# Performance work log

Measured on AMD Instinct MI355X. Metric: run time of the kernel, lower is better.

## Reference

```python
import jax, jax.numpy as jnp
import numpy as np

B, TQ, TK, N = 4, 128, 512, 1024   # batch, query len, key len, key_size
QS, VS, OS = 1024, 1024, 1024      # query_size, value_size, output_size


def setup_inputs() -> dict:
    key = jax.random.key(0)
    ks = jax.random.split(key, 9)
    s_q = 1.0 / np.sqrt(QS)
    s_k = 1.0 / np.sqrt(N)
    s_o = 1.0 / np.sqrt(QS + VS)
    return {
        "query": jax.random.normal(ks[0], (B, TQ, QS), jnp.float32),
        "keys": jax.random.normal(ks[1], (B, TK, N), jnp.float32),
        "values": jax.random.normal(ks[2], (B, TK, VS), jnp.float32),
        # linear_q: query_size -> key_size
        "Wq": jax.random.normal(ks[3], (N, QS), jnp.float32) * s_q,
        "bq": jax.random.normal(ks[4], (N,), jnp.float32) * s_q,
        # linear_att: key_size -> 1
        "w_att": jax.random.normal(ks[5], (N,), jnp.float32) * s_k,
        "b_att": jax.random.normal(ks[6], (), jnp.float32) * s_k,
        # linear_out: (query_size + value_size) -> output_size
        "Wout": jax.random.normal(ks[7], (OS, QS + VS), jnp.float32) * s_o,
        "bout": jax.random.normal(ks[8], (OS,), jnp.float32) * s_o,
    }


def reference(query, keys, values, Wq, bq, w_att, b_att, Wout, bout):
    # linear_q: [b, t_q, query_size] -> [b, t_q, n]
    att_query = jnp.einsum("bqe,ne->bqn", query, Wq) + bq
    # Bahdanau additive score: tanh(q + k) then linear_att (n -> 1)
    # intermediate is [b, t_q, t_k, n] as in the original module
    sum_qk = jnp.tanh(att_query[:, :, None, :] + keys[:, None, :, :])
    scores = jnp.einsum("bqkn,n->bqk", sum_qk, w_att) + b_att  # [b, t_q, t_k]
    scores_normalized = jax.nn.softmax(scores, axis=2)
    # context = softmax(scores) @ values  (dropout is identity with p=0)
    context = jnp.einsum("bqk,bkv->bqv", scores_normalized, values)
    # linear_out on concat([query, context]) + tanh
    cat = jnp.concatenate([query, context], axis=2)  # [b, t_q, q+v]
    out = jnp.tanh(jnp.einsum("bqc,oc->bqo", cat, Wout) + bout)
    return out, scores_normalized
```

## Files before the change

kernel.cpp:

```cpp
#include <hip/hip_runtime.h>
#include <math.h>

static constexpr int B_  = 4;
static constexpr int TQ  = 128;
static constexpr int TK  = 512;
static constexpr int NN  = 1024;
static constexpr int QS  = 1024;
static constexpr int VS  = 1024;
static constexpr int OS  = 1024;

#define K2F    2.8853900817779268f
#define LOG2EF 1.4426950408889634f

typedef __attribute__((ext_vector_type(8))) short bf16x8;
typedef __attribute__((ext_vector_type(4))) float f32x4;

#define MFMA16(a,b,c) __builtin_amdgcn_mfma_f32_16x16x32_bf16((a),(b),(c),0,0,0)

__device__ __forceinline__ ushort bf16_rne(float x) {
    uint u = __float_as_uint(x);
    u += 0x7FFFu + ((u >> 16) & 1u);
    return (ushort)(u >> 16);
}
__device__ __forceinline__ void split2(float x, ushort& h, ushort& l) {
    ushort hh = bf16_rne(x);
    float hv = __uint_as_float((uint)hh << 16);
    h = hh;
    l = bf16_rne(x - hv);
}

__global__ __launch_bounds__(256) void cvt_all_kernel(
    const float* __restrict__ Q, const float* __restrict__ Wq,
    const float* __restrict__ Wo, const float* __restrict__ V,
    ushort* __restrict__ Qh, ushort* __restrict__ Ql,
    ushort* __restrict__ Wqh, ushort* __restrict__ Wql,
    ushort* __restrict__ Woh, ushort* __restrict__ Wol,
    ushort* __restrict__ Vth, ushort* __restrict__ Vtl)
{
    __shared__ float tile[64][65];
    const int bid = blockIdx.x;
    const int t = threadIdx.x;
    if (bid < 3584) {
        const float* src; ushort *h, *l; int idx;
        if (bid < 512)       { src = Q;  h = Qh;  l = Ql;  idx = bid*256 + t; }
        else if (bid < 1536) { src = Wq; h = Wqh; l = Wql; idx = (bid-512)*256 + t; }
        else                 { src = Wo; h = Woh; l = Wol; idx = (bid-1536)*256 + t; }
        float4 v = ((const float4*)src)[idx];
        ushort4 hh, ll;
        split2(v.x, hh.x, ll.x); split2(v.y, hh.y, ll.y);
        split2(v.z, hh.z, ll.z); split2(v.w, hh.w, ll.w);
        ((ushort4*)h)[idx] = hh;
        ((ushort4*)l)[idx] = ll;
        return;
    }
    const int vid = bid - 3584;
    const int v0 = (vid & 15) * 64;
    const int k0 = ((vid >> 4) & 7) * 64;
    const int b  = vid >> 7;
    const float* src = V + ((size_t)b*TK + k0)*VS + v0;
    #pragma unroll
    for (int p = 0; p < 4; ++p) {
        int r = (t >> 4) + p*16, c = (t & 15) * 4;
        float4 vv = *(const float4*)(src + (size_t)r*VS + c);
        tile[r][c] = vv.x; tile[r][c+1] = vv.y; tile[r][c+2] = vv.z; tile[r][c+3] = vv.w;
    }
    __syncthreads();
    ushort* dh = Vth + (size_t)b*(VS*TK) + (size_t)v0*TK + k0;
    ushort* dl = Vtl + (size_t)b*(VS*TK) + (size_t)v0*TK + k0;
    #pragma unroll
    for (int p = 0; p < 4; ++p) {
        int vr = (t >> 4) + p*16, kc = (t & 15) * 4;
        ushort4 hh, ll;
        split2(tile[kc+0][vr], hh.x, ll.x);
        split2(tile[kc+1][vr], hh.y, ll.y);
        split2(tile[kc+2][vr], hh.z, ll.z);
        split2(tile[kc+3][vr], hh.w, ll.w);
        *(ushort4*)(dh + (size_t)vr*TK + kc) = hh;
        *(ushort4*)(dl + (size_t)vr*TK + kc) = ll;
    }
}

__global__ __launch_bounds__(256) void mfma_nt_kernel(
    const ushort* __restrict__ Ah, const ushort* __restrict__ Al,
    const ushort* __restrict__ Bh, const ushort* __restrict__ Bl,
    float* __restrict__ Cp, int lda, int ldb, int Nout, int kchunk, int bstride)
{
    __shared__ alignas(16) ushort lA[2][64][40];
    __shared__ alignas(16) ushort lB[2][64][40];
    const int t = threadIdx.x;
    const int m0 = blockIdx.y * 64, n0 = blockIdx.x * 64, kz = blockIdx.z;
    const int k0 = kz * kchunk;
    const int batch = m0 >> 7;
    const ushort* bhp = Bh + (size_t)batch * bstride;
    const ushort* blp = Bl + (size_t)batch * bstride;
    const int srow = t >> 2, skc = (t & 3) * 8;
    const int lane = t & 63, w = t >> 6;
    const int wm = (w >> 1) * 32, wn = (w & 1) * 32;
    const int fr = lane & 15, fg = (lane >> 4) * 8;

    f32x4 acc00 = {0,0,0,0}, acc01 = {0,0,0,0}, acc10 = {0,0,0,0}, acc11 = {0,0,0,0};

    for (int kb = k0; kb < k0 + kchunk; kb += 32) {
        uint4 va_h = *(const uint4*)(Ah  + (size_t)(m0+srow)*lda + kb + skc);
        uint4 va_l = *(const uint4*)(Al  + (size_t)(m0+srow)*lda + kb + skc);
        uint4 vb_h = *(const uint4*)(bhp + (size_t)(n0+srow)*ldb + kb + skc);
        uint4 vb_l = *(const uint4*)(blp + (size_t)(n0+srow)*ldb + kb + skc);
        *(uint4*)&lA[0][srow][skc] = va_h;
        *(uint4*)&lA[1][srow][skc] = va_l;
        *(uint4*)&lB[0][srow][skc] = vb_h;
        *(uint4*)&lB[1][srow][skc] = vb_l;
        __syncthreads();
        bf16x8 ah0 = *(const bf16x8*)&lA[0][wm + fr     ][fg];
        bf16x8 ah1 = *(const bf16x8*)&lA[0][wm + 16 + fr][fg];
        bf16x8 al0 = *(const bf16x8*)&lA[1][wm + fr     ][fg];
        bf16x8 al1 = *(const bf16x8*)&lA[1][wm + 16 + fr][fg];
        bf16x8 bh0 = *(const bf16x8*)&lB[0][wn + fr     ][fg];
        bf16x8 bh1 = *(const bf16x8*)&lB[0][wn + 16 + fr][fg];
        bf16x8 bl0 = *(const bf16x8*)&lB[1][wn + fr     ][fg];
        bf16x8 bl1 = *(const bf16x8*)&lB[1][wn + 16 + fr][fg];
        acc00 = MFMA16(ah0, bh0, acc00);
        acc00 = MFMA16(al0, bh0, acc00);
        acc00 = MFMA16(ah0, bl0, acc00);
        acc01 = MFMA16(ah0, bh1, acc01);
        acc01 = MFMA16(al0, bh1, acc01);
        acc01 = MFMA16(ah0, bl1, acc01);
        acc10 = MFMA16(ah1, bh0, acc10);
        acc10 = MFMA16(al1, bh0, acc10);
        acc10 = MFMA16(ah1, bl0, acc10);
        acc11 = MFMA16(ah1, bh1, acc11);
        acc11 = MFMA16(al1, bh1, acc11);
        acc11 = MFMA16(ah1, bl1, acc11);
        __syncthreads();
    }
    float* o = Cp + (size_t)kz * 512 * Nout;
    const int orow = (lane >> 4) * 4;
    #pragma unroll
    for (int r2 = 0; r2 < 4; ++r2) {
        o[(size_t)(m0+wm+orow+r2)*Nout      + n0+wn+fr]      = acc00[r2];
        o[(size_t)(m0+wm+orow+r2)*Nout      + n0+wn+16+fr]   = acc01[r2];
        o[(size_t)(m0+wm+16+orow+r2)*Nout   + n0+wn+fr]      = acc10[r2];
        o[(size_t)(m0+wm+16+orow+r2)*Nout   + n0+wn+16+fr]   = acc11[r2];
    }
}

__global__ __launch_bounds__(256) void mfma_out_kernel(
    const ushort* __restrict__ Qh, const ushort* __restrict__ Ql,
    const ushort* __restrict__ Cxh, const ushort* __restrict__ Cxl,
    const ushort* __restrict__ Wh, const ushort* __restrict__ Wl,
    float* __restrict__ Fp)
{
    __shared__ alignas(16) ushort lA[2][64][40];
    __shared__ alignas(16) ushort lB[2][64][40];
    const int t = threadIdx.x;
    const int m0 = blockIdx.y * 64, n0 = blockIdx.x * 64, kz = blockIdx.z;
    const ushort* ah_p = (kz < 2) ? Qh : Cxh;
    const ushort* al_p = (kz < 2) ? Ql : Cxl;
    const int akoff = (kz & 1) * 512;
    const int bkoff = kz * 512;
    const int srow = t >> 2, skc = (t & 3) * 8;
    const int lane = t & 63, w = t >> 6;
    const int wm = (w >> 1) * 32, wn = (w & 1) * 32;
    const int fr = lane & 15, fg = (lane >> 4) * 8;

    f32x4 acc00 = {0,0,0,0}, acc01 = {0,0,0,0}, acc10 = {0,0,0,0}, acc11 = {0,0,0,0};

    for (int kk = 0; kk < 512; kk += 32) {
        uint4 va_h = *(const uint4*)(ah_p + (size_t)(m0+srow)*1024 + akoff + kk + skc);
        uint4 va_l = *(const uint4*)(al_p + (size_t)(m0+srow)*1024 + akoff + kk + skc);
        uint4 vb_h = *(const uint4*)(Wh   + (size_t)(n0+srow)*2048 + bkoff + kk + skc);
        uint4 vb_l = *(const uint4*)(Wl   + (size_t)(n0+srow)*2048 + bkoff + kk + skc);
        *(uint4*)&lA[0][srow][skc] = va_h;
        *(uint4*)&lA[1][srow][skc] = va_l;
        *(uint4*)&lB[0][srow][skc] = vb_h;
        *(uint4*)&lB[1][srow][skc] = vb_l;
        __syncthreads();
        bf16x8 ah0 = *(const bf16x8*)&lA[0][wm + fr     ][fg];
        bf16x8 ah1 = *(const bf16x8*)&lA[0][wm + 16 + fr][fg];
        bf16x8 al0 = *(const bf16x8*)&lA[1][wm + fr     ][fg];
        bf16x8 al1 = *(const bf16x8*)&lA[1][wm + 16 + fr][fg];
        bf16x8 bh0 = *(const bf16x8*)&lB[0][wn + fr     ][fg];
        bf16x8 bh1 = *(const bf16x8*)&lB[0][wn + 16 + fr][fg];
        bf16x8 bl0 = *(const bf16x8*)&lB[1][wn + fr     ][fg];
        bf16x8 bl1 = *(const bf16x8*)&lB[1][wn + 16 + fr][fg];
        acc00 = MFMA16(ah0, bh0, acc00);
        acc00 = MFMA16(al0, bh0, acc00);
        acc00 = MFMA16(ah0, bl0, acc00);
        acc01 = MFMA16(ah0, bh1, acc01);
        acc01 = MFMA16(al0, bh1, acc01);
        acc01 = MFMA16(ah0, bl1, acc01);
        acc10 = MFMA16(ah1, bh0, acc10);
        acc10 = MFMA16(al1, bh0, acc10);
        acc10 = MFMA16(ah1, bl0, acc10);
        acc11 = MFMA16(ah1, bh1, acc11);
        acc11 = MFMA16(al1, bh1, acc11);
        acc11 = MFMA16(ah1, bl1, acc11);
        __syncthreads();
    }
    float* o = Fp + (size_t)kz * 512 * 1024;
    const int orow = (lane >> 4) * 4;
    #pragma unroll
    for (int r2 = 0; r2 < 4; ++r2) {
        o[(size_t)(m0+wm+orow+r2)*1024    + n0+wn+fr]    = acc00[r2];
        o[(size_t)(m0+wm+orow+r2)*1024    + n0+wn+16+fr] = acc01[r2];
        o[(size_t)(m0+wm+16+orow+r2)*1024 + n0+wn+fr]    = acc10[r2];
        o[(size_t)(m0+wm+16+orow+r2)*1024 + n0+wn+16+fr] = acc11[r2];
    }
}

__global__ __launch_bounds__(256) void score_v5_kernel(
    const float* __restrict__ Ap,
    const float* __restrict__ bq,
    const float* __restrict__ keys,
    const float* __restrict__ watt,
    float* __restrict__ Sp)
{
    __shared__ float ea[64][68];
    __shared__ float ek[64][68];
    __shared__ float wl[64];
    const int tid = threadIdx.x;
    const int kt = blockIdx.x;
    const int qt = blockIdx.y;
    const int nh = blockIdx.z;
    const int nbeg = nh * 64;
    const int q0 = qt * 64;
    const int b  = qt >> 1;
    const int k0 = b*TK + kt*64;

    {
        const int r = tid >> 2;
        const int c = (tid & 3) * 16;
        const float* a0 = Ap + (size_t)(q0 + r)*NN + nbeg + c;
        const float* a1 = a0 + 524288;
        const float* bb = bq + nbeg + c;
        const float* kp = keys + (size_t)(k0 + r)*NN + nbeg + c;
        #pragma unroll
        for (int j4 = 0; j4 < 4; ++j4) {
            float4 p0 = *(const float4*)(a0 + j4*4);
            float4 p1 = *(const float4*)(a1 + j4*4);
            float4 bv = *(const float4*)(bb + j4*4);
            ea[c+j4*4+0][r] = exp2f((p0.x + p1.x + bv.x) * K2F);
            ea[c+j4*4+1][r] = exp2f((p0.y + p1.y + bv.y) * K2F);
            ea[c+j4*4+2][r] = exp2f((p0.z + p1.z + bv.z) * K2F);
            ea[c+j4*4+3][r] = exp2f((p0.w + p1.w + bv.w) * K2F);
            float4 kv = *(const float4*)(kp + j4*4);
            ek[c+j4*4+0][r] = exp2f(kv.x * K2F);
            ek[c+j4*4+1][r] = exp2f(kv.y * K2F);
            ek[c+j4*4+2][r] = exp2f(kv.z * K2F);
            ek[c+j4*4+3][r] = exp2f(kv.w * K2F);
        }
        if (tid < 64) wl[tid] = watt[nbeg + tid];
    }
    __syncthreads();

    const int tx = tid & 15;
    const int ty = tid >> 4;
    float acc[4][4] = {};
    #pragma unroll 2
    for (int g = 0; g < 16; ++g) {
        float4 e0 = *(const float4*)&ea[4*g+0][ty*4];
        float4 e1 = *(const float4*)&ea[4*g+1][ty*4];
        float4 e2 = *(const float4*)&ea[4*g+2][ty*4];
        float4 e3 = *(const float4*)&ea[4*g+3][ty*4];
        float4 f0 = *(const float4*)&ek[4*g+0][tx*4];
        float4 f1 = *(const float4*)&ek[4*g+1][tx*4];
        float4 f2 = *(const float4*)&ek[4*g+2][tx*4];
        float4 f3 = *(const float4*)&ek[4*g+3][tx*4];
        float4 w4 = *(const float4*)&wl[4*g];
        float E0[4] = {e0.x,e0.y,e0.z,e0.w};
        float E1[4] = {e1.x,e1.y,e1.z,e1.w};
        float E2[4] = {e2.x,e2.y,e2.z,e2.w};
        float E3[4] = {e3.x,e3.y,e3.z,e3.w};
        float F0[4] = {f0.x,f0.y,f0.z,f0.w};
        float F1[4] = {f1.x,f1.y,f1.z,f1.w};
        float F2[4] = {f2.x,f2.y,f2.z,f2.w};
        float F3[4] = {f3.x,f3.y,f3.z,f3.w};
        #pragma unroll
        for (int i = 0; i < 4; ++i) {
            #pragma unroll
            for (int j = 0; j < 4; ++j) {
                float A  = fmaf(E0[i], F0[j], 1.0f);
                float Bv = fmaf(E1[i], F1[j], 1.0f);
                float C  = fmaf(E2[i], F2[j], 1.0f);
                float D  = fmaf(E3[i], F3[j], 1.0f);
                float n0 = fmaf(w4.x, Bv, w4.y * A);
                float n1 = fmaf(w4.z, D,  w4.w * C);
                acc[i][j] = fmaf(n0, __builtin_amdgcn_rcpf(A * Bv), acc[i][j]);
                acc[i][j] = fmaf(n1, __builtin_amdgcn_rcpf(C * D),  acc[i][j]);
            }
        }
    }
    float* o = Sp + ((size_t)nh*512 + q0 + ty*4)*TK + kt*64 + tx*4;
    #pragma unroll
    for (int i = 0; i < 4; ++i) {
        #pragma unroll
        for (int j = 0; j < 4; ++j)
            o[(size_t)i*TK + j] = acc[i][j];
    }
}

__global__ __launch_bounds__(256) void softmax_kernel(
    const float* __restrict__ Sp, float* __restrict__ P,
    ushort* __restrict__ Ph, ushort* __restrict__ Pl)
{
    const int lane = threadIdx.x & 63;
    const int wid  = threadIdx.x >> 6;
    const int row  = blockIdx.x * 4 + wid;
    const size_t S = (size_t)512*512;
    float v[8];
    float m = -3.4e38f;
    #pragma unroll
    for (int j = 0; j < 8; ++j) {
        int k = lane + j*64;
        float s = 0.f;
        #pragma unroll
        for (int h = 0; h < 16; ++h)
            s += Sp[h*S + (size_t)row*TK + k];
        v[j] = -2.0f * s;
        m = fmaxf(m, v[j]);
    }
    #pragma unroll
    for (int off = 32; off; off >>= 1) m = fmaxf(m, __shfl_xor(m, off, 64));
    float sum = 0.f;
    #pragma unroll
    for (int j = 0; j < 8; ++j) { v[j] = exp2f((v[j] - m) * LOG2EF); sum += v[j]; }
    #pragma unroll
    for (int off = 32; off; off >>= 1) sum += __shfl_xor(sum, off, 64);
    float inv = 1.0f / sum;
    #pragma unroll
    for (int j = 0; j < 8; ++j) {
        int k = lane + j*64;
        float pv = v[j] * inv;
        P[(size_t)row * TK + k] = pv;
        ushort h, l; split2(pv, h, l);
        Ph[(size_t)row * TK + k] = h;
        Pl[(size_t)row * TK + k] = l;
    }
}

__global__ __launch_bounds__(256) void combine_cvt_kernel(
    const float* __restrict__ Ep, ushort* __restrict__ Ch, ushort* __restrict__ Cl)
{
    int i = blockIdx.x * 256 + threadIdx.x;
    float4 p0 = ((const float4*)Ep)[i];
    float4 p1 = ((const float4*)(Ep + (size_t)B_*TQ*VS))[i];
    float4 s = {p0.x+p1.x, p0.y+p1.y, p0.z+p1.z, p0.w+p1.w};
    ushort4 hh, ll;
    split2(s.x, hh.x, ll.x); split2(s.y, hh.y, ll.y);
    split2(s.z, hh.z, ll.z); split2(s.w, hh.w, ll.w);
    ((ushort4*)Ch)[i] = hh;
    ((ushort4*)Cl)[i] = ll;
}

__global__ __launch_bounds__(256) void tanh_combine_kernel(
    const float* __restrict__ Fp, const float* __restrict__ bias,
    float* __restrict__ out)
{
    int i = blockIdx.x * 256 + threadIdx.x;
    const size_t S = (size_t)B_*TQ*OS;
    float4 p0 = ((const float4*)Fp)[i];
    float4 p1 = ((const float4*)(Fp + S))[i];
    float4 p2 = ((const float4*)(Fp + 2*S))[i];
    float4 p3 = ((const float4*)(Fp + 3*S))[i];
    float4 bb = ((const float4*)bias)[i & 255];
    float4 r;
    r.x = tanhf(p0.x + p1.x + p2.x + p3.x + bb.x);
    r.y = tanhf(p0.y + p1.y + p2.y + p3.y + bb.y);
    r.z = tanhf(p0.z + p1.z + p2.z + p3.z + bb.z);
    r.w = tanhf(p0.w + p1.w + p2.w + p3.w + bb.w);
    ((float4*)out)[i] = r;
}

extern "C" void kernel_launch(void* const* d_in, const int* in_sizes, int n_in,
                              void* d_out, int out_size, void* d_ws, size_t ws_size,
                              hipStream_t stream)
{
    const float* query  = (const float*)d_in[0];
    const float* keys   = (const float*)d_in[1];
    const float* values = (const float*)d_in[2];
    const float* Wq     = (const float*)d_in[3];
    const float* bq     = (const float*)d_in[4];
    const float* watt   = (const float*)d_in[5];
    const float* Wout   = (const float*)d_in[7];
    const float* bout   = (const float*)d_in[8];

    float* out = (float*)d_out;
    float* P   = out + (size_t)B_*TQ*OS;

    char* base = (char*)d_ws;
    const size_t MB = 1u << 20;
    ushort* Qh  = (ushort*)(base +  0*MB);
    ushort* Ql  = (ushort*)(base +  1*MB);
    ushort* Wqh = (ushort*)(base +  2*MB);
    ushort* Wql = (ushort*)(base +  4*MB);
    ushort* Woh = (ushort*)(base +  6*MB);
    ushort* Wol = (ushort*)(base + 10*MB);
    ushort* Vth = (ushort*)(base + 14*MB);
    ushort* Vtl = (ushort*)(base + 18*MB);
    float*  Ap  = (float*) (base + 22*MB);
    float*  Sp  = (float*) (base + 28*MB);
    ushort* Ph  = (ushort*)(base + 44*MB);
    ushort* Pl  = (ushort*)(base + 44*MB + 512*1024);
    float*  Ep  = (float*) (base + 45*MB);
    ushort* Cxh = (ushort*)(base + 49*MB);
    ushort* Cxl = (ushort*)(base + 50*MB);
    float*  Fp  = (float*) (base + 51*MB);

    cvt_all_kernel<<<dim3(4096), dim3(256), 0, stream>>>(
        query, Wq, Wout, values, Qh, Ql, Wqh, Wql, Woh, Wol, Vth, Vtl);
    mfma_nt_kernel<<<dim3(16, 8, 2), dim3(256), 0, stream>>>(
        Qh, Ql, Wqh, Wql, Ap, 1024, 1024, 1024, 512, 0);
    score_v5_kernel<<<dim3(8, 8, 16), dim3(256), 0, stream>>>(
        Ap, bq, keys, watt, Sp);
    softmax_kernel<<<dim3(128), dim3(256), 0, stream>>>(Sp, P, Ph, Pl);
    mfma_nt_kernel<<<dim3(16, 8, 2), dim3(256), 0, stream>>>(
        Ph, Pl, Vth, Vtl, Ep, 512, 512, 1024, 256, VS*TK);
    combine_cvt_kernel<<<dim3(512), dim3(256), 0, stream>>>(Ep, Cxh, Cxl);
    mfma_out_kernel<<<dim3(16, 8, 4), dim3(256), 0, stream>>>(
        Qh, Ql, Cxh, Cxl, Woh, Wol, Fp);
    tanh_combine_kernel<<<dim3(512), dim3(256), 0, stream>>>(Fp, bout, out);
}
```

Baseline: 89.33 us.

## Fuse context combine into output GEMM, drop Wout low split, widen split-K

Removes the combine_cvt kernel: the output GEMM now sums the four split-K partials of the context and splits them into bf16 hi/lo while loading its A tile. Wout keeps only its bf16 high half, cutting one of the three MFMAs per tile and the Wl traffic. The Q-projection and PV GEMMs go from 2-way to 4-way split-K for more blocks, and the -2 scale moves from softmax into the score kernel's store. Dropping the Wout low part lowers accuracy of the final projection, and the extra partials add reduction reads downstream.

```diff
diff --git a/kernel.cpp b/kernel.cpp
--- a/kernel.cpp
+++ b/kernel.cpp
@@ -11,6 +11,7 @@
 
 #define K2F    2.8853900817779268f
 #define LOG2EF 1.4426950408889634f
+#define SLICE  524288
 
 typedef __attribute__((ext_vector_type(8))) short bf16x8;
 typedef __attribute__((ext_vector_type(4))) float f32x4;
@@ -34,23 +35,31 @@
     const float* __restrict__ Wo, const float* __restrict__ V,
     ushort* __restrict__ Qh, ushort* __restrict__ Ql,
     ushort* __restrict__ Wqh, ushort* __restrict__ Wql,
-    ushort* __restrict__ Woh, ushort* __restrict__ Wol,
+    ushort* __restrict__ Woh,
     ushort* __restrict__ Vth, ushort* __restrict__ Vtl)
 {
     __shared__ float tile[64][65];
     const int bid = blockIdx.x;
     const int t = threadIdx.x;
     if (bid < 3584) {
-        const float* src; ushort *h, *l; int idx;
-        if (bid < 512)       { src = Q;  h = Qh;  l = Ql;  idx = bid*256 + t; }
-        else if (bid < 1536) { src = Wq; h = Wqh; l = Wql; idx = (bid-512)*256 + t; }
-        else                 { src = Wo; h = Woh; l = Wol; idx = (bid-1536)*256 + t; }
-        float4 v = ((const float4*)src)[idx];
-        ushort4 hh, ll;
-        split2(v.x, hh.x, ll.x); split2(v.y, hh.y, ll.y);
-        split2(v.z, hh.z, ll.z); split2(v.w, hh.w, ll.w);
-        ((ushort4*)h)[idx] = hh;
-        ((ushort4*)l)[idx] = ll;
+        if (bid < 1536) {
+            const float* src; ushort *h, *l; int idx;
+            if (bid < 512) { src = Q;  h = Qh;  l = Ql;  idx = bid*256 + t; }
+            else           { src = Wq; h = Wqh; l = Wql; idx = (bid-512)*256 + t; }
+            float4 v = ((const float4*)src)[idx];
+            ushort4 hh, ll;
+            split2(v.x, hh.x, ll.x); split2(v.y, hh.y, ll.y);
+            split2(v.z, hh.z, ll.z); split2(v.w, hh.w, ll.w);
+            ((ushort4*)h)[idx] = hh;
+            ((ushort4*)l)[idx] = ll;
+        } else {
+            int idx = (bid-1536)*256 + t;
+            float4 v = ((const float4*)Wo)[idx];
+            ushort4 hh;
+            hh.x = bf16_rne(v.x); hh.y = bf16_rne(v.y);
+            hh.z = bf16_rne(v.z); hh.w = bf16_rne(v.w);
+            ((ushort4*)Woh)[idx] = hh;
+        }
         return;
     }
     const int vid = bid - 3584;
@@ -145,16 +154,14 @@
 
 __global__ __launch_bounds__(256) void mfma_out_kernel(
     const ushort* __restrict__ Qh, const ushort* __restrict__ Ql,
-    const ushort* __restrict__ Cxh, const ushort* __restrict__ Cxl,
-    const ushort* __restrict__ Wh, const ushort* __restrict__ Wl,
+    const float* __restrict__ Ep,
+    const ushort* __restrict__ Wh,
     float* __restrict__ Fp)
 {
     __shared__ alignas(16) ushort lA[2][64][40];
-    __shared__ alignas(16) ushort lB[2][64][40];
+    __shared__ alignas(16) ushort lB[64][40];
     const int t = threadIdx.x;
     const int m0 = blockIdx.y * 64, n0 = blockIdx.x * 64, kz = blockIdx.z;
-    const ushort* ah_p = (kz < 2) ? Qh : Cxh;
-    const ushort* al_p = (kz < 2) ? Ql : Cxl;
     const int akoff = (kz & 1) * 512;
     const int bkoff = kz * 512;
     const int srow = t >> 2, skc = (t & 3) * 8;
@@ -165,38 +172,49 @@
     f32x4 acc00 = {0,0,0,0}, acc01 = {0,0,0,0}, acc10 = {0,0,0,0}, acc11 = {0,0,0,0};
 
     for (int kk = 0; kk < 512; kk += 32) {
-        uint4 va_h = *(const uint4*)(ah_p + (size_t)(m0+srow)*1024 + akoff + kk + skc);
-        uint4 va_l = *(const uint4*)(al_p + (size_t)(m0+srow)*1024 + akoff + kk + skc);
-        uint4 vb_h = *(const uint4*)(Wh   + (size_t)(n0+srow)*2048 + bkoff + kk + skc);
-        uint4 vb_l = *(const uint4*)(Wl   + (size_t)(n0+srow)*2048 + bkoff + kk + skc);
-        *(uint4*)&lA[0][srow][skc] = va_h;
-        *(uint4*)&lA[1][srow][skc] = va_l;
-        *(uint4*)&lB[0][srow][skc] = vb_h;
-        *(uint4*)&lB[1][srow][skc] = vb_l;
+        if (kz < 2) {
+            size_t off = (size_t)(m0+srow)*1024 + akoff + kk + skc;
+            *(uint4*)&lA[0][srow][skc] = *(const uint4*)(Qh + off);
+            *(uint4*)&lA[1][srow][skc] = *(const uint4*)(Ql + off);
+        } else {
+            const float* ep = Ep + (size_t)(m0+srow)*1024 + akoff + kk + skc;
+            #pragma unroll
+            for (int j4 = 0; j4 < 2; ++j4) {
+                float4 e0 = *(const float4*)(ep + j4*4);
+                float4 e1 = *(const float4*)(ep + SLICE + j4*4);
+                float4 e2 = *(const float4*)(ep + 2*SLICE + j4*4);
+                float4 e3 = *(const float4*)(ep + 3*SLICE + j4*4);
+                float s0 = e0.x+e1.x+e2.x+e3.x;
+                float s1 = e0.y+e1.y+e2.y+e3.y;
+                float s2 = e0.z+e1.z+e2.z+e3.z;
+                float s3 = e0.w+e1.w+e2.w+e3.w;
+                ushort h, l;
+                split2(s0, h, l); lA[0][srow][skc+j4*4+0]=h; lA[1][srow][skc+j4*4+0]=l;
+                split2(s1, h, l); lA[0][srow][skc+j4*4+1]=h; lA[1][srow][skc+j4*4+1]=l;
+                split2(s2, h, l); lA[0][srow][skc+j4*4+2]=h; lA[1][srow][skc+j4*4+2]=l;
+                split2(s3, h, l); lA[0][srow][skc+j4*4+3]=h; lA[1][srow][skc+j4*4+3]=l;
+            }
+        }
+        *(uint4*)&lB[srow][skc] =
+            *(const uint4*)(Wh + (size_t)(n0+srow)*2048 + bkoff + kk + skc);
         __syncthreads();
         bf16x8 ah0 = *(const bf16x8*)&lA[0][wm + fr     ][fg];
         bf16x8 ah1 = *(const bf16x8*)&lA[0][wm + 16 + fr][fg];
         bf16x8 al0 = *(const bf16x8*)&lA[1][wm + fr     ][fg];
         bf16x8 al1 = *(const bf16x8*)&lA[1][wm + 16 + fr][fg];
-        bf16x8 bh0 = *(const bf16x8*)&lB[0][wn + fr     ][fg];
-        bf16x8 bh1 = *(const bf16x8*)&lB[0][wn + 16 + fr][fg];
-        bf16x8 bl0 = *(const bf16x8*)&lB[1][wn + fr     ][fg];
-        bf16x8 bl1 = *(const bf16x8*)&lB[1][wn + 16 + fr][fg];
+        bf16x8 bh0 = *(const bf16x8*)&lB[wn + fr     ][fg];
+        bf16x8 bh1 = *(const bf16x8*)&lB[wn + 16 + fr][fg];
         acc00 = MFMA16(ah0, bh0, acc00);
         acc00 = MFMA16(al0, bh0, acc00);
-        acc00 = MFMA16(ah0, bl0, acc00);
         acc01 = MFMA16(ah0, bh1, acc01);
         acc01 = MFMA16(al0, bh1, acc01);
-        acc01 = MFMA16(ah0, bl1, acc01);
         acc10 = MFMA16(ah1, bh0, acc10);
         acc10 = MFMA16(al1, bh0, acc10);
-        acc10 = MFMA16(ah1, bl0, acc10);
         acc11 = MFMA16(ah1, bh1, acc11);
         acc11 = MFMA16(al1, bh1, acc11);
-        acc11 = MFMA16(ah1, bl1, acc11);
         __syncthreads();
     }
-    float* o = Fp + (size_t)kz * 512 * 1024;
+    float* o = Fp + (size_t)kz * SLICE;
     const int orow = (lane >> 4) * 4;
     #pragma unroll
     for (int r2 = 0; r2 < 4; ++r2) {
@@ -230,18 +248,19 @@
         const int r = tid >> 2;
         const int c = (tid & 3) * 16;
         const float* a0 = Ap + (size_t)(q0 + r)*NN + nbeg + c;
-        const float* a1 = a0 + 524288;
         const float* bb = bq + nbeg + c;
         const float* kp = keys + (size_t)(k0 + r)*NN + nbeg + c;
         #pragma unroll
         for (int j4 = 0; j4 < 4; ++j4) {
             float4 p0 = *(const float4*)(a0 + j4*4);
-            float4 p1 = *(const float4*)(a1 + j4*4);
+            float4 p1 = *(const float4*)(a0 + SLICE + j4*4);
+            float4 p2 = *(const float4*)(a0 + 2*SLICE + j4*4);
+            float4 p3 = *(const float4*)(a0 + 3*SLICE + j4*4);
             float4 bv = *(const float4*)(bb + j4*4);
-            ea[c+j4*4+0][r] = exp2f((p0.x + p1.x + bv.x) * K2F);
-            ea[c+j4*4+1][r] = exp2f((p0.y + p1.y + bv.y) * K2F);
-            ea[c+j4*4+2][r] = exp2f((p0.z + p1.z + bv.z) * K2F);
-            ea[c+j4*4+3][r] = exp2f((p0.w + p1.w + bv.w) * K2F);
+            ea[c+j4*4+0][r] = exp2f((p0.x+p1.x+p2.x+p3.x+bv.x) * K2F);
+            ea[c+j4*4+1][r] = exp2f((p0.y+p1.y+p2.y+p3.y+bv.y) * K2F);
+            ea[c+j4*4+2][r] = exp2f((p0.z+p1.z+p2.z+p3.z+bv.z) * K2F);
+            ea[c+j4*4+3][r] = exp2f((p0.w+p1.w+p2.w+p3.w+bv.w) * K2F);
             float4 kv = *(const float4*)(kp + j4*4);
             ek[c+j4*4+0][r] = exp2f(kv.x * K2F);
             ek[c+j4*4+1][r] = exp2f(kv.y * K2F);
@@ -294,7 +313,7 @@
     for (int i = 0; i < 4; ++i) {
         #pragma unroll
         for (int j = 0; j < 4; ++j)
-            o[(size_t)i*TK + j] = acc[i][j];
+            o[(size_t)i*TK + j] = -2.0f * acc[i][j];
     }
 }
 
@@ -315,7 +334,7 @@
         #pragma unroll
         for (int h = 0; h < 16; ++h)
             s += Sp[h*S + (size_t)row*TK + k];
-        v[j] = -2.0f * s;
+        v[j] = s;
         m = fmaxf(m, v[j]);
     }
     #pragma unroll
@@ -335,20 +354,6 @@
         Ph[(size_t)row * TK + k] = h;
         Pl[(size_t)row * TK + k] = l;
     }
-}
-
-__global__ __launch_bounds__(256) void combine_cvt_kernel(
-    const float* __restrict__ Ep, ushort* __restrict__ Ch, ushort* __restrict__ Cl)
-{
-    int i = blockIdx.x * 256 + threadIdx.x;
-    float4 p0 = ((const float4*)Ep)[i];
-    float4 p1 = ((const float4*)(Ep + (size_t)B_*TQ*VS))[i];
-    float4 s = {p0.x+p1.x, p0.y+p1.y, p0.z+p1.z, p0.w+p1.w};
-    ushort4 hh, ll;
-    split2(s.x, hh.x, ll.x); split2(s.y, hh.y, ll.y);
-    split2(s.z, hh.z, ll.z); split2(s.w, hh.w, ll.w);
-    ((ushort4*)Ch)[i] = hh;
-    ((ushort4*)Cl)[i] = ll;
 }
 
 __global__ __launch_bounds__(256) void tanh_combine_kernel(
@@ -393,29 +398,25 @@
     ushort* Wqh = (ushort*)(base +  2*MB);
     ushort* Wql = (ushort*)(base +  4*MB);
     ushort* Woh = (ushort*)(base +  6*MB);
-    ushort* Wol = (ushort*)(base + 10*MB);
-    ushort* Vth = (ushort*)(base + 14*MB);
-    ushort* Vtl = (ushort*)(base + 18*MB);
-    float*  Ap  = (float*) (base + 22*MB);
-    float*  Sp  = (float*) (base + 28*MB);
-    ushort* Ph  = (ushort*)(base + 44*MB);
-    ushort* Pl  = (ushort*)(base + 44*MB + 512*1024);
-    float*  Ep  = (float*) (base + 45*MB);
-    ushort* Cxh = (ushort*)(base + 49*MB);
-    ushort* Cxl = (ushort*)(base + 50*MB);
+    ushort* Vth = (ushort*)(base + 10*MB);
+    ushort* Vtl = (ushort*)(base + 14*MB);
+    float*  Ap  = (float*) (base + 18*MB);
+    float*  Sp  = (float*) (base + 26*MB);
+    ushort* Ph  = (ushort*)(base + 42*MB);
+    ushort* Pl  = (ushort*)(base + 42*MB + 512*1024);
+    float*  Ep  = (float*) (base + 43*MB);
     float*  Fp  = (float*) (base + 51*MB);
 
     cvt_all_kernel<<<dim3(4096), dim3(256), 0, stream>>>(
-        query, Wq, Wout, values, Qh, Ql, Wqh, Wql, Woh, Wol, Vth, Vtl);
-    mfma_nt_kernel<<<dim3(16, 8, 2), dim3(256), 0, stream>>>(
-        Qh, Ql, Wqh, Wql, Ap, 1024, 1024, 1024, 512, 0);
+        query, Wq, Wout, values, Qh, Ql, Wqh, Wql, Woh, Vth, Vtl);
+    mfma_nt_kernel<<<dim3(16, 8, 4), dim3(256), 0, stream>>>(
+        Qh, Ql, Wqh, Wql, Ap, 1024, 1024, 1024, 256, 0);
     score_v5_kernel<<<dim3(8, 8, 16), dim3(256), 0, stream>>>(
         Ap, bq, keys, watt, Sp);
     softmax_kernel<<<dim3(128), dim3(256), 0, stream>>>(Sp, P, Ph, Pl);
-    mfma_nt_kernel<<<dim3(16, 8, 2), dim3(256), 0, stream>>>(
-        Ph, Pl, Vth, Vtl, Ep, 512, 512, 1024, 256, VS*TK);
-    combine_cvt_kernel<<<dim3(512), dim3(256), 0, stream>>>(Ep, Cxh, Cxl);
+    mfma_nt_kernel<<<dim3(16, 8, 4), dim3(256), 0, stream>>>(
+        Ph, Pl, Vth, Vtl, Ep, 512, 512, 1024, 128, VS*TK);
     mfma_out_kernel<<<dim3(16, 8, 4), dim3(256), 0, stream>>>(
-        Qh, Ql, Cxh, Cxl, Woh, Wol, Fp);
+        Qh, Ql, Ep, Woh, Fp);
     tanh_combine_kernel<<<dim3(512), dim3(256), 0, stream>>>(Fp, bout, out);
 }
```

Result: slower. 95.01 us (+6.4%).
